# Performance work log

Measured on AMD Instinct MI355X. Metric: run time of the kernel, lower is better.

Reference implementation:

```python
import jax, jax.numpy as jnp
import numpy as np

N_NODES = 100000
N_EDGES = 1600000
IN_CH = 500
H1, C1 = 8, 8           # layer 1: 8 heads x 8 dims, concat -> 64
H2, C2 = 8, 3           # layer 2: 8 heads x 3 classes, mean over heads
NEG_SLOPE = 0.2         # PyG GATConv default


def gat_layer(x, src, dst, W, a_src, a_dst, b, concat):
    """PyG-style GATConv (self-loops already included in src/dst)."""
    N = x.shape[0]
    H, C = a_src.shape
    xw = (x @ W).reshape(N, H, C)                      # [N,H,C]
    al_src = jnp.einsum('nhc,hc->nh', xw, a_src)       # [N,H]
    al_dst = jnp.einsum('nhc,hc->nh', xw, a_dst)       # [N,H]
    e = jax.nn.leaky_relu(al_src[src] + al_dst[dst], NEG_SLOPE)  # [E,H]
    # segment softmax over incoming edges of each destination node
    m = jax.lax.stop_gradient(jax.ops.segment_max(e, dst, num_segments=N))
    ex = jnp.exp(e - m[dst])
    s = jax.ops.segment_sum(ex, dst, num_segments=N)
    alpha = ex / (s[dst] + 1e-16)                      # [E,H]
    out = jax.ops.segment_sum(alpha[:, :, None] * xw[src], dst, num_segments=N)  # [N,H,C]
    out = out.reshape(N, H * C) if concat else out.mean(axis=1)
    return out + b


def setup_inputs() -> dict:
    key = jax.random.key(0)
    ks = jax.random.split(key, 10)
    x = jax.random.normal(ks[0], (N_NODES, IN_CH), dtype=jnp.float32)
    edge_index = jax.random.randint(ks[1], (2, N_EDGES), 0, N_NODES, dtype=jnp.int64)
    sc1 = 1.0 / np.sqrt(IN_CH)
    sc2 = 1.0 / np.sqrt(H1 * C1)
    W1 = jax.random.normal(ks[2], (IN_CH, H1 * C1), dtype=jnp.float32) * sc1
    a1_src = jax.random.normal(ks[3], (H1, C1), dtype=jnp.float32) * 0.1
    a1_dst = jax.random.normal(ks[4], (H1, C1), dtype=jnp.float32) * 0.1
    b1 = jnp.zeros((H1 * C1,), dtype=jnp.float32)
    W2 = jax.random.normal(ks[5], (H1 * C1, H2 * C2), dtype=jnp.float32) * sc2
    a2_src = jax.random.normal(ks[6], (H2, C2), dtype=jnp.float32) * 0.1
    a2_dst = jax.random.normal(ks[7], (H2, C2), dtype=jnp.float32) * 0.1
    b2 = jnp.zeros((C2,), dtype=jnp.float32)
    return {"x": x, "W1": W1, "a1_src": a1_src, "a1_dst": a1_dst, "b1": b1,
            "W2": W2, "a2_src": a2_src, "a2_dst": a2_dst, "b2": b2,
            "edge_index": edge_index}


def reference(x, W1, a1_src, a1_dst, b1, W2, a2_src, a2_dst, b2, edge_index):
    N = x.shape[0]
    loop = jnp.arange(N, dtype=edge_index.dtype)   # PyG add_self_loops=True
    src = jnp.concatenate([edge_index[0], loop])
    dst = jnp.concatenate([edge_index[1], loop])
    h = jax.nn.elu(gat_layer(x, src, dst, W1, a1_src, a1_dst, b1, concat=True))
    out = gat_layer(h, src, dst, W2, a2_src, a2_dst, b2, concat=False)
    return jax.nn.softmax(out, axis=1)
```

## Files before the change

### kernel.cpp

```cpp
#include <hip/hip_runtime.h>
#include <hip/hip_fp16.h>
#include <math.h>

#define N_NODESC 100000
#define N_EDGESC 1600000
#define E_TOT    1700000
#define IN_CH    500
#define KPAD     512
#define D1 64
#define D2 24
#define D2P 32
#define NBKT 391
#define CAP  5120
#define EPB  4096
#define NPB  416
#define GEMB 3125

typedef __attribute__((ext_vector_type(8))) short short8;
typedef __attribute__((ext_vector_type(4))) float f32x4;

__device__ inline short f2bf(float f) {
    unsigned u = __float_as_uint(f);
    u += 0x7fffu + ((u >> 16) & 1u);
    return (short)(u >> 16);
}
__device__ inline unsigned pkbf(float a, float b) {
    const unsigned ua = __float_as_uint(a) + 0x8000u;
    const unsigned ub = __float_as_uint(b) + 0x8000u;
    return __builtin_amdgcn_perm(ub, ua, 0x07060302u);
}
__device__ inline float bflo(unsigned u) { return __uint_as_float(u << 16); }
__device__ inline float bfhi(unsigned u) { return __uint_as_float(u & 0xffff0000u); }

__global__ __launch_bounds__(256) void k_init(int* __restrict__ gcnt,
                                              const float* __restrict__ W1,
                                              short* __restrict__ wT) {
    const int tid = blockIdx.x * 256 + threadIdx.x;
    for (int i = tid; i < D1 * KPAD; i += 16384) {
        const int n = i >> 9, k = i & (KPAD - 1);
        wT[i] = (k < IN_CH) ? f2bf(W1[k * D1 + n]) : (short)0;
    }
    for (int i = tid; i < NBKT * 32; i += 16384) gcnt[i] = 0;
}

__global__ __launch_bounds__(256) void k_pg(const int* __restrict__ ei,
                                            int* __restrict__ gcnt,
                                            int* __restrict__ tmp,
                                            const float* __restrict__ x,
                                            const short* __restrict__ wT,
                                            const float* __restrict__ a1s,
                                            const float* __restrict__ a1d,
                                            short* __restrict__ xw1b,
                                            float* __restrict__ al1s,
                                            float* __restrict__ al1d) {
    __shared__ short xs[32 * 520];
    const int t = threadIdx.x;

    if (blockIdx.x < NPB) {
        int* hist  = (int*)xs;
        int* lbase = hist + NBKT;
        const int e0 = blockIdx.x * EPB;
        for (int i = t; i < NBKT; i += 256) hist[i] = 0;
        __syncthreads();
        int se[16], de[16], mo[16];
#pragma unroll
        for (int i = 0; i < 16; i++) {
            const int e = e0 + i * 256 + t;
            int s = -1, d = 0;
            if (e < E_TOT) {
                if (e < N_EDGESC) { s = ei[e]; d = ei[N_EDGESC + e]; }
                else { s = d = e - N_EDGESC; }
            }
            se[i] = s; de[i] = d;
            mo[i] = (s >= 0) ? atomicAdd(&hist[d >> 8], 1) : 0;
        }
        __syncthreads();
        for (int i = t; i < NBKT; i += 256)
            lbase[i] = hist[i] ? (i * CAP + atomicAdd(&gcnt[i * 32], hist[i])) : 0;
        __syncthreads();
#pragma unroll
        for (int i = 0; i < 16; i++) {
            if (se[i] >= 0) {
                const int b = de[i] >> 8;
                const int idx = lbase[b] + mo[i];
                if (idx < (b + 1) * CAP)
                    tmp[idx] = se[i] | ((de[i] & 255) << 17);
            }
        }
        return;
    }

    const int rowBase = (blockIdx.x - NPB) * 32;
    const int r = t >> 3, j = t & 7;
    const float* xr = x + (long)(rowBase + r) * IN_CH;
    short* xrow = xs + r * 520;
#pragma unroll
    for (int i = 0; i < 16; i++) {
        const int c = j + i * 8;
        if (c < 125) {
            const float4 v = *(const float4*)(xr + c * 4);
            const unsigned lo = pkbf(v.x, v.y);
            const unsigned hi = pkbf(v.z, v.w);
            *(uint2*)(xrow + c * 4) = make_uint2(lo, hi);
        }
    }
    if (j < 6) *(unsigned*)(xrow + 500 + j * 2) = 0u;
    __syncthreads();

    const int lane = t & 63, wv = t >> 6;
    const int m = lane & 15, kg = lane >> 4;
    f32x4 acc[2];
    acc[0] = (f32x4){0.f, 0.f, 0.f, 0.f};
    acc[1] = (f32x4){0.f, 0.f, 0.f, 0.f};
    const short* wcol = wT + (wv * 16 + m) * KPAD;
#pragma unroll
    for (int k0 = 0; k0 < KPAD; k0 += 32) {
        const short8 bf = *(const short8*)(wcol + k0 + kg * 8);
#pragma unroll
        for (int mf = 0; mf < 2; mf++) {
            const short8 af = *(const short8*)(xs + (mf * 16 + m) * 520 + k0 + kg * 8);
            acc[mf] = __builtin_amdgcn_mfma_f32_16x16x32_bf16(af, bf, acc[mf], 0, 0, 0);
        }
    }
    const int col = wv * 16 + m;
    const float as = a1s[col];
    const float ad = a1d[col];
    const int hh = wv * 2 + (m >> 3);
#pragma unroll
    for (int mf = 0; mf < 2; mf++) {
#pragma unroll
        for (int jj = 0; jj < 4; jj++) {
            const int row = rowBase + mf * 16 + kg * 4 + jj;
            const float v = acc[mf][jj];
            xw1b[(long)row * D1 + col] = f2bf(v);
            float ts = v * as, td = v * ad;
            ts += __shfl_xor(ts, 1, 64); td += __shfl_xor(td, 1, 64);
            ts += __shfl_xor(ts, 2, 64); td += __shfl_xor(td, 2, 64);
            ts += __shfl_xor(ts, 4, 64); td += __shfl_xor(td, 4, 64);
            if ((m & 7) == 0) {
                al1s[row * 8 + hh] = ts;
                al1d[row * 8 + hh] = td;
            }
        }
    }
}

__global__ __launch_bounds__(512) void k_bucket2(const int* __restrict__ gcnt,
                                                 const int* __restrict__ tmp,
                                                 int* __restrict__ off,
                                                 int* __restrict__ srt) {
    __shared__ int se[CAP];
    __shared__ int cnts[256];
    __shared__ int sc[256];
    __shared__ int lcur[256];
    __shared__ int red[8];
    __shared__ int sbase;
    const int b = blockIdx.x;
    const int t = threadIdx.x;
    const int cnt = min(gcnt[b * 32], CAP);

    int pre = (t < b) ? min(gcnt[t * 32], CAP) : 0;
#pragma unroll
    for (int m = 1; m < 64; m <<= 1) pre += __shfl_xor(pre, m, 64);
    if ((t & 63) == 0) red[t >> 6] = pre;
    if (t < 256) cnts[t] = 0;
    __syncthreads();
    if (t == 0) {
        int sb = 0;
#pragma unroll
        for (int i = 0; i < 8; i++) sb += red[i];
        sbase = sb;
    }
    __syncthreads();
    const int base = sbase;

    for (int i = t; i < cnt; i += 512) {
        const int p = tmp[b * CAP + i];
        se[i] = p;
        atomicAdd(&cnts[p >> 17], 1);
    }
    __syncthreads();
    if (t < 256) sc[t] = cnts[t];
    __syncthreads();
    for (int d = 1; d < 256; d <<= 1) {
        const int u = (t >= d && t < 256) ? sc[t - d] : 0;
        __syncthreads();
        if (t < 256) sc[t] += u;
        __syncthreads();
    }
    const int nodeBase = b << 8;
    const int nNodes = min(256, N_NODESC - nodeBase);
    if (t < 256) {
        const int excl = base + sc[t] - cnts[t];
        if (t < nNodes) off[nodeBase + t] = excl;
        lcur[t] = excl;
    }
    if (b == 0 && t == 0) off[N_NODESC] = E_TOT;
    __syncthreads();
    for (int i = t; i < cnt; i += 512) {
        const int p = se[i];
        const int pos = atomicAdd(&lcur[p >> 17], 1);
        srt[pos] = p & 0x1FFFF;
    }
}

__global__ __launch_bounds__(512) void k_gat1(const int* __restrict__ off,
                                              const int* __restrict__ srt_src,
                                              const float* __restrict__ al1s,
                                              const float* __restrict__ al1d,
                                              const short* __restrict__ xw1b,
                                              const float* __restrict__ b1,
                                              const float* __restrict__ W2,
                                              const float* __restrict__ a2s,
                                              const float* __restrict__ a2d,
                                              __half* __restrict__ xw2h,
                                              float* __restrict__ al2d) {
    __shared__ float w2s[D1 * D2];
    __shared__ float hrow[8][D1];
    const int tid = threadIdx.x;
    for (int i = tid; i < D1 * D2; i += 512) w2s[i] = W2[i];

    const int lane = tid & 63;
    const int wid = tid >> 6;
    const int n = blockIdx.x * 8 + wid;
    const int e8 = lane >> 3;
    const int hd = lane & 7;

    const float ald = al1d[n * 8 + hd];
    const int kbeg = off[n], kend = off[n + 1];

    float4 a0 = make_float4(0.f, 0.f, 0.f, 0.f);
    float4 a1 = make_float4(0.f, 0.f, 0.f, 0.f);
    float ssum = 0.f;
    int k = kbeg + e8;
    const int s0 = (k      < kend) ? srt_src[k]      : -1;
    const int s1 = (k + 8  < kend) ? srt_src[k + 8]  : -1;
    const int s2 = (k + 16 < kend) ? srt_src[k + 16] : -1;
    float l0 = 0.f, l1 = 0.f, l2 = 0.f;
    uint4 v0 = make_uint4(0u, 0u, 0u, 0u);
    uint4 v1 = make_uint4(0u, 0u, 0u, 0u);
    uint4 v2 = make_uint4(0u, 0u, 0u, 0u);
    if (s0 >= 0) { l0 = al1s[s0 * 8 + hd]; v0 = *(const uint4*)(xw1b + (long)s0 * D1 + hd * 8); }
    if (s1 >= 0) { l1 = al1s[s1 * 8 + hd]; v1 = *(const uint4*)(xw1b + (long)s1 * D1 + hd * 8); }
    if (s2 >= 0) { l2 = al1s[s2 * 8 + hd]; v2 = *(const uint4*)(xw1b + (long)s2 * D1 + hd * 8); }
    if (s0 >= 0) {
        float ev = l0 + ald; ev = ev > 0.f ? ev : 0.2f * ev;
        const float ex = __expf(ev);
        a0.x += ex * bflo(v0.x); a0.y += ex * bfhi(v0.x);
        a0.z += ex * bflo(v0.y); a0.w += ex * bfhi(v0.y);
        a1.x += ex * bflo(v0.z); a1.y += ex * bfhi(v0.z);
        a1.z += ex * bflo(v0.w); a1.w += ex * bfhi(v0.w);
        ssum += ex;
    }
    if (s1 >= 0) {
        float ev = l1 + ald; ev = ev > 0.f ? ev : 0.2f * ev;
        const float ex = __expf(ev);
        a0.x += ex * bflo(v1.x); a0.y += ex * bfhi(v1.x);
        a0.z += ex * bflo(v1.y); a0.w += ex * bfhi(v1.y);
        a1.x += ex * bflo(v1.z); a1.y += ex * bfhi(v1.z);
        a1.z += ex * bflo(v1.w); a1.w += ex * bfhi(v1.w);
        ssum += ex;
    }
    if (s2 >= 0) {
        float ev = l2 + ald; ev = ev > 0.f ? ev : 0.2f * ev;
        const float ex = __expf(ev);
        a0.x += ex * bflo(v2.x); a0.y += ex * bfhi(v2.x);
        a0.z += ex * bflo(v2.y); a0.w += ex * bfhi(v2.y);
        a1.x += ex * bflo(v2.z); a1.y += ex * bfhi(v2.z);
        a1.z += ex * bflo(v2.w); a1.w += ex * bfhi(v2.w);
        ssum += ex;
    }
    for (k = kbeg + 24 + e8; k < kend; k += 8) {
        const int s = srt_src[k];
        const float al = al1s[s * 8 + hd];
        const uint4 v = *(const uint4*)(xw1b + (long)s * D1 + hd * 8);
        float ev = al + ald; ev = ev > 0.f ? ev : 0.2f * ev;
        const float ex = __expf(ev);
        a0.x += ex * bflo(v.x); a0.y += ex * bfhi(v.x);
        a0.z += ex * bflo(v.y); a0.w += ex * bfhi(v.y);
        a1.x += ex * bflo(v.z); a1.y += ex * bfhi(v.z);
        a1.z += ex * bflo(v.w); a1.w += ex * bfhi(v.w);
        ssum += ex;
    }
#pragma unroll
    for (int mm = 8; mm < 64; mm <<= 1) {
        a0.x += __shfl_xor(a0.x, mm, 64); a0.y += __shfl_xor(a0.y, mm, 64);
        a0.z += __shfl_xor(a0.z, mm, 64); a0.w += __shfl_xor(a0.w, mm, 64);
        a1.x += __shfl_xor(a1.x, mm, 64); a1.y += __shfl_xor(a1.y, mm, 64);
        a1.z += __shfl_xor(a1.z, mm, 64); a1.w += __shfl_xor(a1.w, mm, 64);
        ssum  += __shfl_xor(ssum,  mm, 64);
    }
    const float inv = 1.0f / (ssum + 1e-16f);
    const float4 bb0 = *(const float4*)(b1 + hd * 8);
    const float4 bb1 = *(const float4*)(b1 + hd * 8 + 4);
    float4 r0, r1;
    r0.x = a0.x * inv + bb0.x; r0.x = r0.x > 0.f ? r0.x : expm1f(r0.x);
    r0.y = a0.y * inv + bb0.y; r0.y = r0.y > 0.f ? r0.y : expm1f(r0.y);
    r0.z = a0.z * inv + bb0.z; r0.z = r0.z > 0.f ? r0.z : expm1f(r0.z);
    r0.w = a0.w * inv + bb0.w; r0.w = r0.w > 0.f ? r0.w : expm1f(r0.w);
    r1.x = a1.x * inv + bb1.x; r1.x = r1.x > 0.f ? r1.x : expm1f(r1.x);
    r1.y = a1.y * inv + bb1.y; r1.y = r1.y > 0.f ? r1.y : expm1f(r1.y);
    r1.z = a1.z * inv + bb1.z; r1.z = r1.z > 0.f ? r1.z : expm1f(r1.z);
    r1.w = a1.w * inv + bb1.w; r1.w = r1.w > 0.f ? r1.w : expm1f(r1.w);
    if (e8 == 0) {
        *(float4*)(&hrow[wid][hd * 8])     = r0;
        *(float4*)(&hrow[wid][hd * 8 + 4]) = r1;
    }
    __syncthreads();
    const int half_ = lane / 24;
    const int j2 = lane - half_ * 24;
    const int cb = (half_ == 1) ? 32 : 0;
    float o = 0.f;
#pragma unroll
    for (int c4 = 0; c4 < 8; c4++) {
        const float4 hv = *(const float4*)(&hrow[wid][cb + c4 * 4]);
        const float* wr = w2s + (cb + c4 * 4) * D2 + j2;
        o += hv.x * wr[0] + hv.y * wr[D2] + hv.z * wr[2 * D2] + hv.w * wr[3 * D2];
    }
    const int src2 = (lane < 24) ? lane + 24 : lane;
    o += __shfl(o, src2, 64);
    if (lane < 24) {
        const int h3 = j2 / 3;
        xw2h[(long)n * D2P + h3 * 4 + (j2 - 3 * h3)] = __float2half(o);
    }
    const float ps = o * a2s[j2];
    const float pd = o * a2d[j2];
    const int hb = 3 * (lane & 7);
    const float s3 = __shfl(ps, hb, 64) + __shfl(ps, hb + 1, 64) + __shfl(ps, hb + 2, 64);
    const float d3 = __shfl(pd, hb, 64) + __shfl(pd, hb + 1, 64) + __shfl(pd, hb + 2, 64);
    if (lane < 8) {
        xw2h[(long)n * D2P + lane * 4 + 3] = __float2half(s3);
        al2d[n * 8 + lane] = d3;
    }
}

__global__ __launch_bounds__(256) void k_gat2(const int* __restrict__ off,
                                              const int* __restrict__ srt_src,
                                              const float* __restrict__ al2d,
                                              const __half* __restrict__ xw2h,
                                              const float* __restrict__ b2,
                                              float* __restrict__ out) {
    const int tid = threadIdx.x;
    const int lane = tid & 63;
    const int wid = tid >> 6;
    const int n = blockIdx.x * 4 + wid;
    const int e8 = lane >> 3;
    const int hd = lane & 7;

    const float ald = al2d[n * 8 + hd];
    const int kbeg = off[n], kend = off[n + 1];

    float ax = 0.f, ay = 0.f, az = 0.f, ssum = 0.f;
    int k = kbeg + e8;
    const int s0 = (k      < kend) ? srt_src[k]      : -1;
    const int s1 = (k + 8  < kend) ? srt_src[k + 8]  : -1;
    const int s2 = (k + 16 < kend) ? srt_src[k + 16] : -1;
    uint2 v0 = make_uint2(0u, 0u);
    uint2 v1 = make_uint2(0u, 0u);
    uint2 v2 = make_uint2(0u, 0u);
    if (s0 >= 0) v0 = *(const uint2*)(xw2h + (long)s0 * D2P + hd * 4);
    if (s1 >= 0) v1 = *(const uint2*)(xw2h + (long)s1 * D2P + hd * 4);
    if (s2 >= 0) v2 = *(const uint2*)(xw2h + (long)s2 * D2P + hd * 4);
    if (s0 >= 0) {
        const float2 f0 = __half22float2(*(const __half2*)&v0.x);
        const float2 f1 = __half22float2(*(const __half2*)&v0.y);
        float ev = f1.y + ald; ev = ev > 0.f ? ev : 0.2f * ev;
        const float ex = __expf(ev);
        ax += ex * f0.x; ay += ex * f0.y; az += ex * f1.x; ssum += ex;
    }
    if (s1 >= 0) {
        const float2 f0 = __half22float2(*(const __half2*)&v1.x);
        const float2 f1 = __half22float2(*(const __half2*)&v1.y);
        float ev = f1.y + ald; ev = ev > 0.f ? ev : 0.2f * ev;
        const float ex = __expf(ev);
        ax += ex * f0.x; ay += ex * f0.y; az += ex * f1.x; ssum += ex;
    }
    if (s2 >= 0) {
        const float2 f0 = __half22float2(*(const __half2*)&v2.x);
        const float2 f1 = __half22float2(*(const __half2*)&v2.y);
        float ev = f1.y + ald; ev = ev > 0.f ? ev : 0.2f * ev;
        const float ex = __expf(ev);
        ax += ex * f0.x; ay += ex * f0.y; az += ex * f1.x; ssum += ex;
    }
    for (k = kbeg + 24 + e8; k < kend; k += 8) {
        const int s = srt_src[k];
        const uint2 v = *(const uint2*)(xw2h + (long)s * D2P + hd * 4);
        const float2 f0 = __half22float2(*(const __half2*)&v.x);
        const float2 f1 = __half22float2(*(const __half2*)&v.y);
        float ev = f1.y + ald; ev = ev > 0.f ? ev : 0.2f * ev;
        const float ex = __expf(ev);
        ax += ex * f0.x; ay += ex * f0.y; az += ex * f1.x; ssum += ex;
    }
#pragma unroll
    for (int mm = 8; mm < 64; mm <<= 1) {
        ax += __shfl_xor(ax, mm, 64);
        ay += __shfl_xor(ay, mm, 64);
        az += __shfl_xor(az, mm, 64);
        ssum += __shfl_xor(ssum, mm, 64);
    }
    const float inv = 1.0f / (ssum + 1e-16f);
    float mx = ax * inv, my = ay * inv, mz = az * inv;
#pragma unroll
    for (int mm = 1; mm < 8; mm <<= 1) {
        mx += __shfl_xor(mx, mm, 64);
        my += __shfl_xor(my, mm, 64);
        mz += __shfl_xor(mz, mm, 64);
    }
    const float l0 = mx * 0.125f + b2[0];
    const float l1 = my * 0.125f + b2[1];
    const float l2 = mz * 0.125f + b2[2];
    const float mmax = fmaxf(l0, fmaxf(l1, l2));
    const float ee0 = expf(l0 - mmax), ee1 = expf(l1 - mmax), ee2 = expf(l2 - mmax);
    const float dinv = 1.0f / (ee0 + ee1 + ee2);
    if (lane < 3) {
        const float p = (lane == 0) ? ee0 : (lane == 1) ? ee1 : ee2;
        out[(long)n * 3 + lane] = p * dinv;
    }
}

extern "C" void kernel_launch(void* const* d_in, const int* in_sizes, int n_in,
                              void* d_out, int out_size, void* d_ws, size_t ws_size,
                              hipStream_t stream) {
    const float* x   = (const float*)d_in[0];
    const float* W1  = (const float*)d_in[1];
    const float* a1s = (const float*)d_in[2];
    const float* a1d = (const float*)d_in[3];
    const float* b1  = (const float*)d_in[4];
    const float* W2  = (const float*)d_in[5];
    const float* a2s = (const float*)d_in[6];
    const float* a2d = (const float*)d_in[7];
    const float* b2  = (const float*)d_in[8];
    const int*   ei  = (const int*)d_in[9];
    float* out = (float*)d_out;

    float* ws    = (float*)d_ws;
    float* al1s  = ws;
    float* al1d  = al1s + 800000;
    float* al2d  = al1d + 800000;
    short* xw1b  = (short*)(al2d + 800000);
    __half* xw2h = (__half*)(xw1b + 6400000);
    int* off     = (int*)(xw2h + 3200000);
    int* gcnt    = off + 100004;
    int* srt     = gcnt + NBKT * 32;
    short* wT    = (short*)(srt + 1700000);
    int* tmp     = (int*)(wT + 32768);

    k_init<<<64, 256, 0, stream>>>(gcnt, W1, wT);
    k_pg<<<NPB + GEMB, 256, 0, stream>>>(ei, gcnt, tmp, x, wT, a1s, a1d,
                                         xw1b, al1s, al1d);
    k_bucket2<<<NBKT, 512, 0, stream>>>(gcnt, tmp, off, srt);
    k_gat1<<<N_NODESC / 8, 512, 0, stream>>>(off, srt, al1s, al1d, xw1b, b1,
                                             W2, a2s, a2d, xw2h, al2d);
    k_gat2<<<N_NODESC / 4, 256, 0, stream>>>(off, srt, al2d, xw2h, b2, out);
}
```

Before: 453.0 us.

## Fuse bucket sort into layer-1 aggregation using block-local sorted edges in LDS

Merges the per-bucket counting sort and the layer-1 GAT aggregation into one kernel. Two blocks per 256-node bucket each redo the sort into shared memory, then aggregate their half of the nodes by reading source indices from LDS instead of global memory. One block also writes the global sorted array and offsets for layer 2. Layer 2 moves to 512-thread blocks with 8 nodes each. This saves a launch and the global round-trip for the sorted edges, at the cost of duplicated sort work and only 782 large blocks with heavy LDS use, which may hurt occupancy.

```diff
diff --git a/kernel.cpp b/kernel.cpp
--- a/kernel.cpp
+++ b/kernel.cpp
@@ -145,67 +145,10 @@
     }
 }
 
-__global__ __launch_bounds__(512) void k_bucket2(const int* __restrict__ gcnt,
-                                                 const int* __restrict__ tmp,
-                                                 int* __restrict__ off,
-                                                 int* __restrict__ srt) {
-    __shared__ int se[CAP];
-    __shared__ int cnts[256];
-    __shared__ int sc[256];
-    __shared__ int lcur[256];
-    __shared__ int red[8];
-    __shared__ int sbase;
-    const int b = blockIdx.x;
-    const int t = threadIdx.x;
-    const int cnt = min(gcnt[b * 32], CAP);
-
-    int pre = (t < b) ? min(gcnt[t * 32], CAP) : 0;
-#pragma unroll
-    for (int m = 1; m < 64; m <<= 1) pre += __shfl_xor(pre, m, 64);
-    if ((t & 63) == 0) red[t >> 6] = pre;
-    if (t < 256) cnts[t] = 0;
-    __syncthreads();
-    if (t == 0) {
-        int sb = 0;
-#pragma unroll
-        for (int i = 0; i < 8; i++) sb += red[i];
-        sbase = sb;
-    }
-    __syncthreads();
-    const int base = sbase;
-
-    for (int i = t; i < cnt; i += 512) {
-        const int p = tmp[b * CAP + i];
-        se[i] = p;
-        atomicAdd(&cnts[p >> 17], 1);
-    }
-    __syncthreads();
-    if (t < 256) sc[t] = cnts[t];
-    __syncthreads();
-    for (int d = 1; d < 256; d <<= 1) {
-        const int u = (t >= d && t < 256) ? sc[t - d] : 0;
-        __syncthreads();
-        if (t < 256) sc[t] += u;
-        __syncthreads();
-    }
-    const int nodeBase = b << 8;
-    const int nNodes = min(256, N_NODESC - nodeBase);
-    if (t < 256) {
-        const int excl = base + sc[t] - cnts[t];
-        if (t < nNodes) off[nodeBase + t] = excl;
-        lcur[t] = excl;
-    }
-    if (b == 0 && t == 0) off[N_NODESC] = E_TOT;
-    __syncthreads();
-    for (int i = t; i < cnt; i += 512) {
-        const int p = se[i];
-        const int pos = atomicAdd(&lcur[p >> 17], 1);
-        srt[pos] = p & 0x1FFFF;
-    }
-}
-
-__global__ __launch_bounds__(512) void k_gat1(const int* __restrict__ off,
-                                              const int* __restrict__ srt_src,
+__global__ __launch_bounds__(512) void k_gatA(const int* __restrict__ gcnt,
+                                              const int* __restrict__ tmp,
+                                              int* __restrict__ off,
+                                              int* __restrict__ srt,
                                               const float* __restrict__ al1s,
                                               const float* __restrict__ al1d,
                                               const short* __restrict__ xw1b,
@@ -215,126 +158,181 @@
                                               const float* __restrict__ a2d,
                                               __half* __restrict__ xw2h,
                                               float* __restrict__ al2d) {
+    __shared__ int   srtL[CAP];
+    __shared__ int   cnts[256];
+    __shared__ int   sc[256];
+    __shared__ int   lcur[256];
+    __shared__ int   red[8];
+    __shared__ int   sbase;
     __shared__ float w2s[D1 * D2];
     __shared__ float hrow[8][D1];
-    const int tid = threadIdx.x;
-    for (int i = tid; i < D1 * D2; i += 512) w2s[i] = W2[i];
-
-    const int lane = tid & 63;
-    const int wid = tid >> 6;
-    const int n = blockIdx.x * 8 + wid;
+    const int t = threadIdx.x;
+    const int b = blockIdx.x >> 1;
+    const int h = blockIdx.x & 1;
+    const int cnt = min(gcnt[b * 32], CAP);
+
+    for (int i = t; i < D1 * D2; i += 512) w2s[i] = W2[i];
+
+    int pre = (t < b) ? min(gcnt[t * 32], CAP) : 0;
+#pragma unroll
+    for (int m = 1; m < 64; m <<= 1) pre += __shfl_xor(pre, m, 64);
+    if ((t & 63) == 0) red[t >> 6] = pre;
+    if (t < 256) cnts[t] = 0;
+    __syncthreads();
+    if (t == 0) {
+        int sb = 0;
+#pragma unroll
+        for (int i = 0; i < 8; i++) sb += red[i];
+        sbase = sb;
+    }
+    __syncthreads();
+    const int base = sbase;
+
+    for (int i = t; i < cnt; i += 512)
+        atomicAdd(&cnts[tmp[b * CAP + i] >> 17], 1);
+    __syncthreads();
+    if (t < 256) sc[t] = cnts[t];
+    __syncthreads();
+    for (int d = 1; d < 256; d <<= 1) {
+        const int u = (t >= d && t < 256) ? sc[t - d] : 0;
+        __syncthreads();
+        if (t < 256) sc[t] += u;
+        __syncthreads();
+    }
+    const int nodeBase = b << 8;
+    if (t < 256) {
+        const int excl = sc[t] - cnts[t];
+        lcur[t] = excl;
+        if (h == 0 && nodeBase + t < N_NODESC) off[nodeBase + t] = base + excl;
+    }
+    if (h == 0 && b == 0 && t == 0) off[N_NODESC] = E_TOT;
+    __syncthreads();
+    for (int i = t; i < cnt; i += 512) {
+        const int p = tmp[b * CAP + i];
+        const int pos = atomicAdd(&lcur[p >> 17], 1);
+        const int s = p & 0x1FFFF;
+        srtL[pos] = s;
+        if (h == 0) srt[base + pos] = s;
+    }
+    __syncthreads();
+
+    const int lane = t & 63;
+    const int w = t >> 6;
     const int e8 = lane >> 3;
     const int hd = lane & 7;
 
-    const float ald = al1d[n * 8 + hd];
-    const int kbeg = off[n], kend = off[n + 1];
-
-    float4 a0 = make_float4(0.f, 0.f, 0.f, 0.f);
-    float4 a1 = make_float4(0.f, 0.f, 0.f, 0.f);
-    float ssum = 0.f;
-    int k = kbeg + e8;
-    const int s0 = (k      < kend) ? srt_src[k]      : -1;
-    const int s1 = (k + 8  < kend) ? srt_src[k + 8]  : -1;
-    const int s2 = (k + 16 < kend) ? srt_src[k + 16] : -1;
-    float l0 = 0.f, l1 = 0.f, l2 = 0.f;
-    uint4 v0 = make_uint4(0u, 0u, 0u, 0u);
-    uint4 v1 = make_uint4(0u, 0u, 0u, 0u);
-    uint4 v2 = make_uint4(0u, 0u, 0u, 0u);
-    if (s0 >= 0) { l0 = al1s[s0 * 8 + hd]; v0 = *(const uint4*)(xw1b + (long)s0 * D1 + hd * 8); }
-    if (s1 >= 0) { l1 = al1s[s1 * 8 + hd]; v1 = *(const uint4*)(xw1b + (long)s1 * D1 + hd * 8); }
-    if (s2 >= 0) { l2 = al1s[s2 * 8 + hd]; v2 = *(const uint4*)(xw1b + (long)s2 * D1 + hd * 8); }
-    if (s0 >= 0) {
-        float ev = l0 + ald; ev = ev > 0.f ? ev : 0.2f * ev;
-        const float ex = __expf(ev);
-        a0.x += ex * bflo(v0.x); a0.y += ex * bfhi(v0.x);
-        a0.z += ex * bflo(v0.y); a0.w += ex * bfhi(v0.y);
-        a1.x += ex * bflo(v0.z); a1.y += ex * bfhi(v0.z);
-        a1.z += ex * bflo(v0.w); a1.w += ex * bfhi(v0.w);
-        ssum += ex;
-    }
-    if (s1 >= 0) {
-        float ev = l1 + ald; ev = ev > 0.f ? ev : 0.2f * ev;
-        const float ex = __expf(ev);
-        a0.x += ex * bflo(v1.x); a0.y += ex * bfhi(v1.x);
-        a0.z += ex * bflo(v1.y); a0.w += ex * bfhi(v1.y);
-        a1.x += ex * bflo(v1.z); a1.y += ex * bfhi(v1.z);
-        a1.z += ex * bflo(v1.w); a1.w += ex * bfhi(v1.w);
-        ssum += ex;
-    }
-    if (s2 >= 0) {
-        float ev = l2 + ald; ev = ev > 0.f ? ev : 0.2f * ev;
-        const float ex = __expf(ev);
-        a0.x += ex * bflo(v2.x); a0.y += ex * bfhi(v2.x);
-        a0.z += ex * bflo(v2.y); a0.w += ex * bfhi(v2.y);
-        a1.x += ex * bflo(v2.z); a1.y += ex * bfhi(v2.z);
-        a1.z += ex * bflo(v2.w); a1.w += ex * bfhi(v2.w);
-        ssum += ex;
-    }
-    for (k = kbeg + 24 + e8; k < kend; k += 8) {
-        const int s = srt_src[k];
-        const float al = al1s[s * 8 + hd];
-        const uint4 v = *(const uint4*)(xw1b + (long)s * D1 + hd * 8);
-        float ev = al + ald; ev = ev > 0.f ? ev : 0.2f * ev;
-        const float ex = __expf(ev);
-        a0.x += ex * bflo(v.x); a0.y += ex * bfhi(v.x);
-        a0.z += ex * bflo(v.y); a0.w += ex * bfhi(v.y);
-        a1.x += ex * bflo(v.z); a1.y += ex * bfhi(v.z);
-        a1.z += ex * bflo(v.w); a1.w += ex * bfhi(v.w);
-        ssum += ex;
-    }
-#pragma unroll
-    for (int mm = 8; mm < 64; mm <<= 1) {
-        a0.x += __shfl_xor(a0.x, mm, 64); a0.y += __shfl_xor(a0.y, mm, 64);
-        a0.z += __shfl_xor(a0.z, mm, 64); a0.w += __shfl_xor(a0.w, mm, 64);
-        a1.x += __shfl_xor(a1.x, mm, 64); a1.y += __shfl_xor(a1.y, mm, 64);
-        a1.z += __shfl_xor(a1.z, mm, 64); a1.w += __shfl_xor(a1.w, mm, 64);
-        ssum  += __shfl_xor(ssum,  mm, 64);
-    }
-    const float inv = 1.0f / (ssum + 1e-16f);
-    const float4 bb0 = *(const float4*)(b1 + hd * 8);
-    const float4 bb1 = *(const float4*)(b1 + hd * 8 + 4);
-    float4 r0, r1;
-    r0.x = a0.x * inv + bb0.x; r0.x = r0.x > 0.f ? r0.x : expm1f(r0.x);
-    r0.y = a0.y * inv + bb0.y; r0.y = r0.y > 0.f ? r0.y : expm1f(r0.y);
-    r0.z = a0.z * inv + bb0.z; r0.z = r0.z > 0.f ? r0.z : expm1f(r0.z);
-    r0.w = a0.w * inv + bb0.w; r0.w = r0.w > 0.f ? r0.w : expm1f(r0.w);
-    r1.x = a1.x * inv + bb1.x; r1.x = r1.x > 0.f ? r1.x : expm1f(r1.x);
-    r1.y = a1.y * inv + bb1.y; r1.y = r1.y > 0.f ? r1.y : expm1f(r1.y);
-    r1.z = a1.z * inv + bb1.z; r1.z = r1.z > 0.f ? r1.z : expm1f(r1.z);
-    r1.w = a1.w * inv + bb1.w; r1.w = r1.w > 0.f ? r1.w : expm1f(r1.w);
-    if (e8 == 0) {
-        *(float4*)(&hrow[wid][hd * 8])     = r0;
-        *(float4*)(&hrow[wid][hd * 8 + 4]) = r1;
-    }
-    __syncthreads();
-    const int half_ = lane / 24;
-    const int j2 = lane - half_ * 24;
-    const int cb = (half_ == 1) ? 32 : 0;
-    float o = 0.f;
-#pragma unroll
-    for (int c4 = 0; c4 < 8; c4++) {
-        const float4 hv = *(const float4*)(&hrow[wid][cb + c4 * 4]);
-        const float* wr = w2s + (cb + c4 * 4) * D2 + j2;
-        o += hv.x * wr[0] + hv.y * wr[D2] + hv.z * wr[2 * D2] + hv.w * wr[3 * D2];
-    }
-    const int src2 = (lane < 24) ? lane + 24 : lane;
-    o += __shfl(o, src2, 64);
-    if (lane < 24) {
-        const int h3 = j2 / 3;
-        xw2h[(long)n * D2P + h3 * 4 + (j2 - 3 * h3)] = __float2half(o);
-    }
-    const float ps = o * a2s[j2];
-    const float pd = o * a2d[j2];
-    const int hb = 3 * (lane & 7);
-    const float s3 = __shfl(ps, hb, 64) + __shfl(ps, hb + 1, 64) + __shfl(ps, hb + 2, 64);
-    const float d3 = __shfl(pd, hb, 64) + __shfl(pd, hb + 1, 64) + __shfl(pd, hb + 2, 64);
-    if (lane < 8) {
-        xw2h[(long)n * D2P + lane * 4 + 3] = __float2half(s3);
-        al2d[n * 8 + lane] = d3;
-    }
-}
-
-__global__ __launch_bounds__(256) void k_gat2(const int* __restrict__ off,
+    for (int idx = h * 128 + w; idx < h * 128 + 128 && nodeBase + idx < N_NODESC; idx += 8) {
+        const int n = nodeBase + idx;
+        const int kb = sc[idx] - cnts[idx];
+        const int ke = sc[idx];
+        const float ald = al1d[n * 8 + hd];
+
+        float4 a0 = make_float4(0.f, 0.f, 0.f, 0.f);
+        float4 a1 = make_float4(0.f, 0.f, 0.f, 0.f);
+        float ssum = 0.f;
+        const int k0i = kb + e8;
+        const int s0 = (k0i      < ke) ? srtL[k0i]      : -1;
+        const int s1 = (k0i + 8  < ke) ? srtL[k0i + 8]  : -1;
+        const int s2 = (k0i + 16 < ke) ? srtL[k0i + 16] : -1;
+        float l0 = 0.f, l1 = 0.f, l2 = 0.f;
+        uint4 v0 = make_uint4(0u, 0u, 0u, 0u);
+        uint4 v1 = make_uint4(0u, 0u, 0u, 0u);
+        uint4 v2 = make_uint4(0u, 0u, 0u, 0u);
+        if (s0 >= 0) { l0 = al1s[s0 * 8 + hd]; v0 = *(const uint4*)(xw1b + (long)s0 * D1 + hd * 8); }
+        if (s1 >= 0) { l1 = al1s[s1 * 8 + hd]; v1 = *(const uint4*)(xw1b + (long)s1 * D1 + hd * 8); }
+        if (s2 >= 0) { l2 = al1s[s2 * 8 + hd]; v2 = *(const uint4*)(xw1b + (long)s2 * D1 + hd * 8); }
+        if (s0 >= 0) {
+            float ev = l0 + ald; ev = ev > 0.f ? ev : 0.2f * ev;
+            const float ex = __expf(ev);
+            a0.x += ex * bflo(v0.x); a0.y += ex * bfhi(v0.x);
+            a0.z += ex * bflo(v0.y); a0.w += ex * bfhi(v0.y);
+            a1.x += ex * bflo(v0.z); a1.y += ex * bfhi(v0.z);
+            a1.z += ex * bflo(v0.w); a1.w += ex * bfhi(v0.w);
+            ssum += ex;
+        }
+        if (s1 >= 0) {
+            float ev = l1 + ald; ev = ev > 0.f ? ev : 0.2f * ev;
+            const float ex = __expf(ev);
+            a0.x += ex * bflo(v1.x); a0.y += ex * bfhi(v1.x);
+            a0.z += ex * bflo(v1.y); a0.w += ex * bfhi(v1.y);
+            a1.x += ex * bflo(v1.z); a1.y += ex * bfhi(v1.z);
+            a1.z += ex * bflo(v1.w); a1.w += ex * bfhi(v1.w);
+            ssum += ex;
+        }
+        if (s2 >= 0) {
+            float ev = l2 + ald; ev = ev > 0.f ? ev : 0.2f * ev;
+            const float ex = __expf(ev);
+            a0.x += ex * bflo(v2.x); a0.y += ex * bfhi(v2.x);
+            a0.z += ex * bflo(v2.y); a0.w += ex * bfhi(v2.y);
+            a1.x += ex * bflo(v2.z); a1.y += ex * bfhi(v2.z);
+            a1.z += ex * bflo(v2.w); a1.w += ex * bfhi(v2.w);
+            ssum += ex;
+        }
+        for (int kk = kb + 24 + e8; kk < ke; kk += 8) {
+            const int s = srtL[kk];
+            const float al = al1s[s * 8 + hd];
+            const uint4 v = *(const uint4*)(xw1b + (long)s * D1 + hd * 8);
+            float ev = al + ald; ev = ev > 0.f ? ev : 0.2f * ev;
+            const float ex = __expf(ev);
+            a0.x += ex * bflo(v.x); a0.y += ex * bfhi(v.x);
+            a0.z += ex * bflo(v.y); a0.w += ex * bfhi(v.y);
+            a1.x += ex * bflo(v.z); a1.y += ex * bfhi(v.z);
+            a1.z += ex * bflo(v.w); a1.w += ex * bfhi(v.w);
+            ssum += ex;
+        }
+#pragma unroll
+        for (int mm = 8; mm < 64; mm <<= 1) {
+            a0.x += __shfl_xor(a0.x, mm, 64); a0.y += __shfl_xor(a0.y, mm, 64);
+            a0.z += __shfl_xor(a0.z, mm, 64); a0.w += __shfl_xor(a0.w, mm, 64);
+            a1.x += __shfl_xor(a1.x, mm, 64); a1.y += __shfl_xor(a1.y, mm, 64);
+            a1.z += __shfl_xor(a1.z, mm, 64); a1.w += __shfl_xor(a1.w, mm, 64);
+            ssum  += __shfl_xor(ssum,  mm, 64);
+        }
+        const float inv = 1.0f / (ssum + 1e-16f);
+        const float4 bb0 = *(const float4*)(b1 + hd * 8);
+        const float4 bb1 = *(const float4*)(b1 + hd * 8 + 4);
+        float4 r0, r1;
+        r0.x = a0.x * inv + bb0.x; r0.x = r0.x > 0.f ? r0.x : expm1f(r0.x);
+        r0.y = a0.y * inv + bb0.y; r0.y = r0.y > 0.f ? r0.y : expm1f(r0.y);
+        r0.z = a0.z * inv + bb0.z; r0.z = r0.z > 0.f ? r0.z : expm1f(r0.z);
+        r0.w = a0.w * inv + bb0.w; r0.w = r0.w > 0.f ? r0.w : expm1f(r0.w);
+        r1.x = a1.x * inv + bb1.x; r1.x = r1.x > 0.f ? r1.x : expm1f(r1.x);
+        r1.y = a1.y * inv + bb1.y; r1.y = r1.y > 0.f ? r1.y : expm1f(r1.y);
+        r1.z = a1.z * inv + bb1.z; r1.z = r1.z > 0.f ? r1.z : expm1f(r1.z);
+        r1.w = a1.w * inv + bb1.w; r1.w = r1.w > 0.f ? r1.w : expm1f(r1.w);
+        if (e8 == 0) {
+            *(float4*)(&hrow[w][hd * 8])     = r0;
+            *(float4*)(&hrow[w][hd * 8 + 4]) = r1;
+        }
+        const int half_ = lane / 24;
+        const int j2 = lane - half_ * 24;
+        const int cb = (half_ == 1) ? 32 : 0;
+        float o = 0.f;
+#pragma unroll
+        for (int c4 = 0; c4 < 8; c4++) {
+            const float4 hv = *(const float4*)(&hrow[w][cb + c4 * 4]);
+            const float* wr = w2s + (cb + c4 * 4) * D2 + j2;
+            o += hv.x * wr[0] + hv.y * wr[D2] + hv.z * wr[2 * D2] + hv.w * wr[3 * D2];
+        }
+        const int src2 = (lane < 24) ? lane + 24 : lane;
+        o += __shfl(o, src2, 64);
+        if (lane < 24) {
+            const int h3 = j2 / 3;
+            xw2h[(long)n * D2P + h3 * 4 + (j2 - 3 * h3)] = __float2half(o);
+        }
+        const float ps = o * a2s[j2];
+        const float pd = o * a2d[j2];
+        const int hb = 3 * (lane & 7);
+        const float s3 = __shfl(ps, hb, 64) + __shfl(ps, hb + 1, 64) + __shfl(ps, hb + 2, 64);
+        const float d3 = __shfl(pd, hb, 64) + __shfl(pd, hb + 1, 64) + __shfl(pd, hb + 2, 64);
+        if (lane < 8) {
+            xw2h[(long)n * D2P + lane * 4 + 3] = __float2half(s3);
+            al2d[n * 8 + lane] = d3;
+        }
+    }
+}
+
+__global__ __launch_bounds__(512) void k_gat2(const int* __restrict__ off,
                                               const int* __restrict__ srt_src,
                                               const float* __restrict__ al2d,
                                               const __half* __restrict__ xw2h,
@@ -343,7 +341,7 @@
     const int tid = threadIdx.x;
     const int lane = tid & 63;
     const int wid = tid >> 6;
-    const int n = blockIdx.x * 4 + wid;
+    const int n = blockIdx.x * 8 + wid;
     const int e8 = lane >> 3;
     const int hd = lane & 7;
 
@@ -448,8 +446,7 @@
     k_init<<<64, 256, 0, stream>>>(gcnt, W1, wT);
     k_pg<<<NPB + GEMB, 256, 0, stream>>>(ei, gcnt, tmp, x, wT, a1s, a1d,
                                          xw1b, al1s, al1d);
-    k_bucket2<<<NBKT, 512, 0, stream>>>(gcnt, tmp, off, srt);
-    k_gat1<<<N_NODESC / 8, 512, 0, stream>>>(off, srt, al1s, al1d, xw1b, b1,
-                                             W2, a2s, a2d, xw2h, al2d);
-    k_gat2<<<N_NODESC / 4, 256, 0, stream>>>(off, srt, al2d, xw2h, b2, out);
-}
+    k_gatA<<<NBKT * 2, 512, 0, stream>>>(gcnt, tmp, off, srt, al1s, al1d, xw1b,
+                                         b1, W2, a2s, a2d, xw2h, al2d);
+    k_gat2<<<N_NODESC / 8, 512, 0, stream>>>(off, srt, al2d, xw2h, b2, out);
+}
```

Measured after the change: 467.5 us. 1.03x slower.
